# Performance work log

Measured on AMD Instinct MI355X. Metric: run time of the kernel, lower is better.

Reference implementation:

```python
import jax, jax.numpy as jnp
import numpy as np

K = 10  # top-k per query


def setup_inputs() -> dict:
    key = jax.random.key(0)
    k1, k2 = jax.random.split(key)
    B_Q, B_D = 4096, 32768
    similarity_scores = jax.random.normal(k1, (B_Q, B_D), dtype=jnp.float32)
    positive_mask = jax.random.randint(k2, (B_Q, B_D), 0, 2).astype(jnp.bool_)
    return {"similarity_scores": similarity_scores, "positive_mask": positive_mask}


def reference(similarity_scores, positive_mask):
    # Per-row top-k over the doc axis: values [B,k], indices [B,k]
    top_k_values, top_k_indices = jax.lax.top_k(similarity_scores, K)
    labels = jnp.take_along_axis(
        positive_mask.astype(jnp.float32), top_k_indices, axis=1
    )  # [B, k] relevance labels at the top-k positions

    # DCG discounts: log2(position + 1), positions 1..k
    positions = jnp.arange(1, K + 1, dtype=jnp.float32)
    discounts = jnp.log2(positions + 1.0)  # [k]

    actual_dcg = jnp.sum(labels / discounts, axis=1)  # [B]
    ideal_labels = -jnp.sort(-labels, axis=1)  # descending sort
    ideal_dcg = jnp.sum(ideal_labels / discounts, axis=1)  # [B]

    # Loss per query: 1 - NDCG if ideal_dcg > 0 else 0.
    # (Queries with no positives anywhere also have ideal_dcg == 0 -> skipped,
    #  matching the torch `continue` / early-return-0 behavior.)
    per_query = jnp.where(ideal_dcg > 0, 1.0 - actual_dcg / jnp.maximum(ideal_dcg, 1e-30), 0.0)

    batch_size_query = similarity_scores.shape[0]
    return jnp.sum(per_query) / batch_size_query
```

## Files before the change

### kernel.cpp

```cpp
#include <hip/hip_runtime.h>
#include <cstdint>
#include <cstddef>

#define KTOP 10
#define BQ 4096
#define BD 32768
#define THREADS 256
#define F4_PER_ROW (BD / 4)
#define ITERS (F4_PER_ROW / THREADS)
#define ROWS_PER_BLK 2
#define CAPG 256
#define T_STATIC 3.0f
#define CAP_FUSED 2560

#define WS_COUNTS 16384
#define WS_GVAL   32768
#define WS_REQ (WS_GVAL + (size_t)BQ * CAPG * 8)

__device__ __forceinline__ void insert_tie(float v, int j, float (&tv)[KTOP], int (&ti)[KTOP]) {
    const bool enter = (v > tv[KTOP - 1]) || (v == tv[KTOP - 1] && j < ti[KTOP - 1]);
    if (enter) {
        bool cc[KTOP];
#pragma unroll
        for (int k = 0; k < KTOP; ++k) cc[k] = (v > tv[k]) || (v == tv[k] && j < ti[k]);
#pragma unroll
        for (int k = KTOP - 1; k >= 1; --k) {
            tv[k] = cc[k] ? (cc[k - 1] ? tv[k - 1] : v) : tv[k];
            ti[k] = cc[k] ? (cc[k - 1] ? ti[k - 1] : j) : ti[k];
        }
        if (cc[0]) { tv[0] = v; ti[0] = j; }
    }
}

__device__ __forceinline__ void wave_extract10(float (&tv)[KTOP], int (&ti)[KTOP],
                                               int lane, float &myv, int &myi) {
#pragma unroll
    for (int r = 0; r < KTOP; ++r) {
        float bv = tv[0]; int bi = ti[0]; int bl = lane;
#pragma unroll
        for (int m = 32; m >= 1; m >>= 1) {
            const float ov = __shfl_xor(bv, m);
            const int   oi = __shfl_xor(bi, m);
            const int   ol = __shfl_xor(bl, m);
            const bool take = (ov > bv) || (ov == bv && oi < bi);
            bv = take ? ov : bv;
            bi = take ? oi : bi;
            bl = take ? ol : bl;
        }
        if (lane == bl) {
#pragma unroll
            for (int k = 0; k < KTOP - 1; ++k) { tv[k] = tv[k + 1]; ti[k] = ti[k + 1]; }
            tv[KTOP - 1] = -INFINITY; ti[KTOP - 1] = 0x7fffffff;
        }
        if (lane == r) { myv = bv; myi = bi; }
    }
}

__device__ __forceinline__ void wave_loss(float (&tv)[KTOP], int (&ti)[KTOP], int lane,
                                          const int* __restrict__ mrow, float* __restrict__ dst) {
    float myv = 0.0f; int myi = 0;
    wave_extract10(tv, ti, lane, myv, myi);
    const int pos = (lane < KTOP) ? ((mrow[myi] != 0) ? 1 : 0) : 0;
    int cnt = pos;
#pragma unroll
    for (int m = 32; m >= 1; m >>= 1) cnt += __shfl_xor(cnt, m);
    const float invd = 1.0f / log2f((float)(lane + 2));
    float a = pos ? invd : 0.0f;
    float b = (lane < cnt) ? invd : 0.0f;
#pragma unroll
    for (int m = 32; m >= 1; m >>= 1) { a += __shfl_xor(a, m); b += __shfl_xor(b, m); }
    if (lane == 0) *dst = (b > 0.0f) ? (1.0f - a / b) : 0.0f;
}

__global__ __launch_bounds__(THREADS) void collect_two_rows(
    const float* __restrict__ scores,
    float* __restrict__ gval, int* __restrict__ gidx, int* __restrict__ counts)
{
    const int tid = threadIdx.x;
    __shared__ int s_cnt;
    if (tid == 0) s_cnt = 0;
    __syncthreads();

    for (int rr = 0; rr < ROWS_PER_BLK; ++rr) {
        const int row = blockIdx.x * ROWS_PER_BLK + rr;
        const float4* row4 = reinterpret_cast<const float4*>(scores + (size_t)row * BD);
        float* __restrict__ gv = gval + (size_t)row * CAPG;
        int*   __restrict__ gi = gidx + (size_t)row * CAPG;

        for (int i = 0; i < ITERS; ++i) {
            const int f4 = tid + i * THREADS;
            const float4 x = row4[f4];
            const float m = fmaxf(fmaxf(x.x, x.y), fmaxf(x.z, x.w));
            if (m >= T_STATIC) {
                const int jb = f4 * 4;
                const float vs[4] = { x.x, x.y, x.z, x.w };
#pragma unroll
                for (int c = 0; c < 4; ++c) {
                    if (vs[c] >= T_STATIC) {
                        const int p = atomicAdd(&s_cnt, 1);
                        if (p < CAPG) { gv[p] = vs[c]; gi[p] = jb + c; }
                    }
                }
            }
        }
        __syncthreads();
        if (tid == 0) { counts[row] = s_cnt; s_cnt = 0; }
        __syncthreads();
    }
}

__global__ __launch_bounds__(64) void merge_rows(
    const float* __restrict__ scores, const int* __restrict__ mask,
    const float* __restrict__ gval, const int* __restrict__ gidx,
    const int* __restrict__ counts, float* __restrict__ per_row)
{
    const int row  = blockIdx.x;
    const int lane = threadIdx.x;
    const int n = counts[row];

    float tv[KTOP]; int ti[KTOP];
#pragma unroll
    for (int k = 0; k < KTOP; ++k) { tv[k] = -INFINITY; ti[k] = 0x7fffffff; }

    if (n >= KTOP && n <= CAPG) {
        const float* gv = gval + (size_t)row * CAPG;
        const int*   gi = gidx + (size_t)row * CAPG;
        for (int p = lane; p < n; p += 64) insert_tie(gv[p], gi[p], tv, ti);
    } else {
        const float4* row4 = reinterpret_cast<const float4*>(scores + (size_t)row * BD);
        for (int f4 = lane; f4 < F4_PER_ROW; f4 += 64) {
            const float4 x = row4[f4];
            const int jb = f4 * 4;
            const float vs[4] = { x.x, x.y, x.z, x.w };
#pragma unroll
            for (int c = 0; c < 4; ++c) insert_tie(vs[c], jb + c, tv, ti);
        }
    }
    wave_loss(tv, ti, lane, mask + (size_t)row * BD, per_row + row);
}

__global__ __launch_bounds__(THREADS) void topk_ndcg_fused(
    const float* __restrict__ scores, const int* __restrict__ mask,
    float* __restrict__ per_row)
{
    const int row  = blockIdx.x;
    const int tid  = threadIdx.x;
    const int lane = tid & 63;
    const int wv   = tid >> 6;
    const float4* row4 = reinterpret_cast<const float4*>(scores + (size_t)row * BD);

    __shared__ int   s_cnt;
    __shared__ float cv[CAP_FUSED];
    __shared__ int   ci[CAP_FUSED];
    if (tid == 0) s_cnt = 0;
    __syncthreads();

    for (int i = 0; i < ITERS; ++i) {
        const int f4 = tid + i * THREADS;
        const float4 x = row4[f4];
        const float m = fmaxf(fmaxf(x.x, x.y), fmaxf(x.z, x.w));
        if (m >= T_STATIC) {
            const int jb = f4 * 4;
            const float vs[4] = { x.x, x.y, x.z, x.w };
#pragma unroll
            for (int c = 0; c < 4; ++c) {
                if (vs[c] >= T_STATIC) {
                    const int p = atomicAdd(&s_cnt, 1);
                    if (p < CAP_FUSED) { cv[p] = vs[c]; ci[p] = jb + c; }
                }
            }
        }
    }
    __syncthreads();
    int n = s_cnt;

    float tv[KTOP]; int ti[KTOP];
#pragma unroll
    for (int k = 0; k < KTOP; ++k) { tv[k] = -INFINITY; ti[k] = 0x7fffffff; }

    if (n < KTOP || n > CAP_FUSED) {
        for (int i = 0; i < ITERS; ++i) {
            const int f4 = i * THREADS + tid;
            const float4 x = row4[f4];
            const int jb = f4 * 4;
            const float vs[4] = { x.x, x.y, x.z, x.w };
#pragma unroll
            for (int c = 0; c < 4; ++c) insert_tie(vs[c], jb + c, tv, ti);
        }
        float fv = 0.0f; int fi = 0;
        wave_extract10(tv, ti, lane, fv, fi);
        if (lane < KTOP) { cv[wv * KTOP + lane] = fv; ci[wv * KTOP + lane] = fi; }
        __syncthreads();
        n = 4 * KTOP;
#pragma unroll
        for (int k = 0; k < KTOP; ++k) { tv[k] = -INFINITY; ti[k] = 0x7fffffff; }
    }

    if (wv == 0) {
        for (int p = lane; p < n; p += 64) insert_tie(cv[p], ci[p], tv, ti);
        wave_loss(tv, ti, lane, mask + (size_t)row * BD, per_row + row);
    }
}

__global__ __launch_bounds__(256) void reduce_mean(
    const float* __restrict__ per_row, float* __restrict__ out)
{
    const int tid = threadIdx.x;
    float s = 0.0f;
    for (int i = tid; i < BQ; i += 256) s += per_row[i];
#pragma unroll
    for (int m = 32; m >= 1; m >>= 1) s += __shfl_xor(s, m);
    __shared__ float ws[4];
    if ((tid & 63) == 0) ws[tid >> 6] = s;
    __syncthreads();
    if (tid == 0) out[0] = (ws[0] + ws[1] + ws[2] + ws[3]) / (float)BQ;
}

extern "C" void kernel_launch(void* const* d_in, const int* in_sizes, int n_in,
                              void* d_out, int out_size, void* d_ws, size_t ws_size,
                              hipStream_t stream) {
    const float* scores = (const float*)d_in[0];
    const int*   mask   = (const int*)d_in[1];

    char* ws = (char*)d_ws;
    float* per_row = (float*)ws;
    int*   counts  = (int*)(ws + WS_COUNTS);
    float* gval    = (float*)(ws + WS_GVAL);
    int*   gidx    = (int*)(ws + WS_GVAL + (size_t)BQ * CAPG * 4);

    if (ws_size >= WS_REQ) {
        collect_two_rows<<<BQ / ROWS_PER_BLK, THREADS, 0, stream>>>(scores, gval, gidx, counts);
        merge_rows<<<BQ, 64, 0, stream>>>(scores, mask, gval, gidx, counts, per_row);
    } else {
        topk_ndcg_fused<<<BQ, THREADS, 0, stream>>>(scores, mask, per_row);
    }
    reduce_mean<<<1, 256, 0, stream>>>(per_row, (float*)d_out);
}
```

Baseline: 145.6 us.

## Replace shared-memory atomics with per-wave ballot compaction in candidate collection

The collect kernel now handles one row per block. Each wave compacts its threshold candidates into its own 64-slot region using ballot and mbcnt prefix counts, which removes the LDS atomic and the block-level barriers. Per-wave counts are written out, and the merge kernel walks the four wave regions. A wave that overflows its 64 slots forces a full-row fallback even when the row's total count would have fit, and the launch now uses twice as many blocks.

```diff
diff --git a/kernel.cpp b/kernel.cpp
--- a/kernel.cpp
+++ b/kernel.cpp
@@ -8,14 +8,20 @@
 #define THREADS 256
 #define F4_PER_ROW (BD / 4)
 #define ITERS (F4_PER_ROW / THREADS)
-#define ROWS_PER_BLK 2
-#define CAPG 256
+#define WAVES 4
+#define SLOTS 64
+#define CAPG (WAVES * SLOTS)
 #define T_STATIC 3.0f
 #define CAP_FUSED 2560
 
 #define WS_COUNTS 16384
-#define WS_GVAL   32768
-#define WS_REQ (WS_GVAL + (size_t)BQ * CAPG * 8)
+#define WS_GVAL   (16384 + 65536)
+#define WS_REQ ((size_t)WS_GVAL + (size_t)BQ * CAPG * 8)
+
+__device__ __forceinline__ unsigned prefix_lt(unsigned long long b) {
+    unsigned p = __builtin_amdgcn_mbcnt_lo((unsigned)(b & 0xffffffffull), 0u);
+    return __builtin_amdgcn_mbcnt_hi((unsigned)(b >> 32), p);
+}
 
 __device__ __forceinline__ void insert_tie(float v, int j, float (&tv)[KTOP], int (&ti)[KTOP]) {
     const bool enter = (v > tv[KTOP - 1]) || (v == tv[KTOP - 1] && j < ti[KTOP - 1]);
@@ -72,41 +78,42 @@
     if (lane == 0) *dst = (b > 0.0f) ? (1.0f - a / b) : 0.0f;
 }
 
-__global__ __launch_bounds__(THREADS) void collect_two_rows(
+__global__ __launch_bounds__(THREADS) void collect_rows(
     const float* __restrict__ scores,
     float* __restrict__ gval, int* __restrict__ gidx, int* __restrict__ counts)
 {
-    const int tid = threadIdx.x;
-    __shared__ int s_cnt;
-    if (tid == 0) s_cnt = 0;
-    __syncthreads();
-
-    for (int rr = 0; rr < ROWS_PER_BLK; ++rr) {
-        const int row = blockIdx.x * ROWS_PER_BLK + rr;
-        const float4* row4 = reinterpret_cast<const float4*>(scores + (size_t)row * BD);
-        float* __restrict__ gv = gval + (size_t)row * CAPG;
-        int*   __restrict__ gi = gidx + (size_t)row * CAPG;
-
-        for (int i = 0; i < ITERS; ++i) {
-            const int f4 = tid + i * THREADS;
-            const float4 x = row4[f4];
-            const float m = fmaxf(fmaxf(x.x, x.y), fmaxf(x.z, x.w));
-            if (m >= T_STATIC) {
-                const int jb = f4 * 4;
-                const float vs[4] = { x.x, x.y, x.z, x.w };
-#pragma unroll
-                for (int c = 0; c < 4; ++c) {
-                    if (vs[c] >= T_STATIC) {
-                        const int p = atomicAdd(&s_cnt, 1);
-                        if (p < CAPG) { gv[p] = vs[c]; gi[p] = jb + c; }
+    const int row  = blockIdx.x;
+    const int tid  = threadIdx.x;
+    const int lane = tid & 63;
+    const int wv   = tid >> 6;
+    const float4* row4 = reinterpret_cast<const float4*>(scores + (size_t)row * BD);
+    float* __restrict__ gv = gval + (size_t)row * CAPG + wv * SLOTS;
+    int*   __restrict__ gi = gidx + (size_t)row * CAPG + wv * SLOTS;
+
+    int cnt = 0;
+    for (int i = 0; i < ITERS; ++i) {
+        const int f4 = tid + i * THREADS;
+        const float4 x = row4[f4];
+        const float m = fmaxf(fmaxf(x.x, x.y), fmaxf(x.z, x.w));
+        const unsigned long long any = __ballot(m >= T_STATIC);
+        if (any) {
+            const int jb = f4 * 4;
+            const float vs[4] = { x.x, x.y, x.z, x.w };
+#pragma unroll
+            for (int c = 0; c < 4; ++c) {
+                const bool cand = vs[c] >= T_STATIC;
+                const unsigned long long b = __ballot(cand);
+                if (b) {
+                    if (cand) {
+                        const int slot = cnt + (int)prefix_lt(b);
+                        if (slot < SLOTS) { gv[slot] = vs[c]; gi[slot] = jb + c; }
                     }
+                    cnt += __popcll(b);
                 }
             }
         }
-        __syncthreads();
-        if (tid == 0) { counts[row] = s_cnt; s_cnt = 0; }
-        __syncthreads();
-    }
+    }
+    if (lane == 0) counts[row * WAVES + wv] = cnt;
 }
 
 __global__ __launch_bounds__(64) void merge_rows(
@@ -116,16 +123,25 @@
 {
     const int row  = blockIdx.x;
     const int lane = threadIdx.x;
-    const int n = counts[row];
+    const int c0 = counts[row * WAVES + 0];
+    const int c1 = counts[row * WAVES + 1];
+    const int c2 = counts[row * WAVES + 2];
+    const int c3 = counts[row * WAVES + 3];
+    const bool ok = (c0 <= SLOTS) && (c1 <= SLOTS) && (c2 <= SLOTS) && (c3 <= SLOTS) &&
+                    (c0 + c1 + c2 + c3 >= KTOP);
 
     float tv[KTOP]; int ti[KTOP];
 #pragma unroll
     for (int k = 0; k < KTOP; ++k) { tv[k] = -INFINITY; ti[k] = 0x7fffffff; }
 
-    if (n >= KTOP && n <= CAPG) {
+    if (ok) {
         const float* gv = gval + (size_t)row * CAPG;
         const int*   gi = gidx + (size_t)row * CAPG;
-        for (int p = lane; p < n; p += 64) insert_tie(gv[p], gi[p], tv, ti);
+        const int cw[4] = { c0, c1, c2, c3 };
+#pragma unroll
+        for (int w = 0; w < 4; ++w)
+            for (int p = lane; p < cw[w]; p += 64)
+                insert_tie(gv[w * SLOTS + p], gi[w * SLOTS + p], tv, ti);
     } else {
         const float4* row4 = reinterpret_cast<const float4*>(scores + (size_t)row * BD);
         for (int f4 = lane; f4 < F4_PER_ROW; f4 += 64) {
@@ -229,7 +245,7 @@
     int*   gidx    = (int*)(ws + WS_GVAL + (size_t)BQ * CAPG * 4);
 
     if (ws_size >= WS_REQ) {
-        collect_two_rows<<<BQ / ROWS_PER_BLK, THREADS, 0, stream>>>(scores, gval, gidx, counts);
+        collect_rows<<<BQ, THREADS, 0, stream>>>(scores, gval, gidx, counts);
         merge_rows<<<BQ, 64, 0, stream>>>(scores, mask, gval, gidx, counts, per_row);
     } else {
         topk_ndcg_fused<<<BQ, THREADS, 0, stream>>>(scores, mask, per_row);
```

Result: slower. 168.6 us (+15.8%).
